# Optimization experiments

Hardware: AMD Instinct MI355X
Metric: run time of the kernel (lower is better)

## Reference

```python
import jax, jax.numpy as jnp
import numpy as np

B, S, D, H = 4, 2048, 1024, 16
DK = D // H

def setup_inputs() -> dict:
    key = jax.random.key(0)
    ks = jax.random.split(key, 8)
    scale = 1.0 / np.sqrt(D)
    return {
        "q": jax.random.normal(ks[0], (B, S, D), jnp.float32),
        "k": jax.random.normal(ks[1], (B, S, D), jnp.float32),
        "v": jax.random.normal(ks[2], (B, S, D), jnp.float32),
        "wq": jax.random.normal(ks[3], (D, D), jnp.float32) * scale,
        "bq": jnp.zeros((D,), jnp.float32),
        "wk": jax.random.normal(ks[4], (D, D), jnp.float32) * scale,
        "bk": jnp.zeros((D,), jnp.float32),
        "wv": jax.random.normal(ks[5], (D, D), jnp.float32) * scale,
        "bv": jnp.zeros((D,), jnp.float32),
        "wo": jax.random.normal(ks[6], (D, D), jnp.float32) * scale,
        "bo": jnp.zeros((D,), jnp.float32),
    }

def reference(q, k, v, wq, bq, wk, bk, wv, bv, wo, bo):
    b, s, _ = q.shape
    # projections; split heads -> [b, h, s, d_k]
    def proj(x, w, bias):
        y = x @ w + bias
        return y.reshape(b, -1, H, DK).transpose(0, 2, 1, 3)
    qh, kh, vh = proj(q, wq, bq), proj(k, wk, bk), proj(v, wv, bv)
    scores = jnp.einsum("bhqd,bhkd->bhqk", qh, kh) / np.sqrt(DK).astype(jnp.float32)
    attn = jax.nn.softmax(scores, axis=-1)  # dropout = identity (eval mode)
    out = jnp.einsum("bhqk,bhkd->bhqd", attn, vh)
    out = out.transpose(0, 2, 1, 3).reshape(b, s, D)
    return out @ wo + bo
```

## Files before the change

kernel.cpp:

```cpp
#include <hip/hip_runtime.h>
#include <hip/hip_bf16.h>

#define B_   4
#define S_   2048
#define D_   1024
#define H_   16
#define DK_  64
#define NTOK 8192

typedef __bf16 bf16_t;
typedef __bf16 bf16x8 __attribute__((ext_vector_type(8)));
typedef __bf16 bf16x4 __attribute__((ext_vector_type(4)));
typedef __bf16 bf16x2 __attribute__((ext_vector_type(2)));
typedef float  f32x4  __attribute__((ext_vector_type(4)));
typedef float  f32x16 __attribute__((ext_vector_type(16)));
typedef unsigned u32x4 __attribute__((ext_vector_type(4)));
typedef int    i32x2  __attribute__((ext_vector_type(2)));

__device__ __forceinline__ void gll16(const void* g, void* l) {
  __builtin_amdgcn_global_load_lds(
      (const __attribute__((address_space(1))) void*)g,
      (__attribute__((address_space(3))) void*)l,
      16, 0, 0);
}

__device__ __forceinline__ f32x4 mfma32(bf16x8 a, bf16x8 b, f32x4 c) {
  return __builtin_amdgcn_mfma_f32_16x16x32_bf16(a, b, c, 0, 0, 0);
}

__device__ __forceinline__ f32x16 mfma32x32(bf16x8 a, bf16x8 b, f32x16 c) {
#if defined(__HIP_DEVICE_COMPILE__)
  return __builtin_amdgcn_mfma_f32_32x32x16_bf16(a, b, c, 0, 0, 0);
#else
  (void)a; (void)b;
  return c;
#endif
}

__device__ __forceinline__ float fast_exp2(float x) {
#if defined(__HIP_DEVICE_COMPILE__) && __has_builtin(__builtin_amdgcn_exp2f)
  return __builtin_amdgcn_exp2f(x);
#else
  return exp2f(x);
#endif
}

__device__ __forceinline__ f32x16 zero16() {
  f32x16 z;
#pragma unroll
  for (int i = 0; i < 16; ++i) z[i] = 0.f;
  return z;
}

__device__ __forceinline__ unsigned pkbf(float lo, float hi) {
  bf16x2 t;
  t[0] = (bf16_t)lo;
  t[1] = (bf16_t)hi;
  return __builtin_bit_cast(unsigned, t);
}

__device__ __forceinline__ void plswap(unsigned &x, unsigned &y) {
#if defined(__HIP_DEVICE_COMPILE__)
  i32x2 r = __builtin_amdgcn_permlane32_swap((int)x, (int)y, false, false);
  x = (unsigned)r[0];
  y = (unsigned)r[1];
#endif
}

__device__ __forceinline__ void build_pa(const f32x16 s, bf16x8 &p0, bf16x8 &p1) {
  unsigned A0 = pkbf(fast_exp2(s[0]),  fast_exp2(s[1]));
  unsigned A1 = pkbf(fast_exp2(s[2]),  fast_exp2(s[3]));
  unsigned B0 = pkbf(fast_exp2(s[4]),  fast_exp2(s[5]));
  unsigned B1 = pkbf(fast_exp2(s[6]),  fast_exp2(s[7]));
  unsigned C0 = pkbf(fast_exp2(s[8]),  fast_exp2(s[9]));
  unsigned C1 = pkbf(fast_exp2(s[10]), fast_exp2(s[11]));
  unsigned D0 = pkbf(fast_exp2(s[12]), fast_exp2(s[13]));
  unsigned D1 = pkbf(fast_exp2(s[14]), fast_exp2(s[15]));
  plswap(A0, B0);
  plswap(A1, B1);
  plswap(C0, D0);
  plswap(C1, D1);
  u32x4 lo = {A0, A1, B0, B1};
  u32x4 hi = {C0, C1, D0, D1};
  p0 = __builtin_bit_cast(bf16x8, lo);
  p1 = __builtin_bit_cast(bf16x8, hi);
}

__global__ __launch_bounds__(256) void tobf16(
    const float* __restrict__ q, const float* __restrict__ k,
    const float* __restrict__ v, bf16_t* __restrict__ o) {
  const float* src = (blockIdx.z == 0) ? q : (blockIdx.z == 1) ? k : v;
  bf16_t* dst = o + (size_t)blockIdx.z * 8388608;
  size_t i = ((size_t)blockIdx.x * 256 + threadIdx.x) * 4;
  float4 x = *(const float4*)&src[i];
  bf16x4 y;
  y[0] = (bf16_t)x.x; y[1] = (bf16_t)x.y;
  y[2] = (bf16_t)x.z; y[3] = (bf16_t)x.w;
  *(bf16x4*)&dst[i] = y;
}

__global__ __launch_bounds__(256) void prep_weights(
    const float* __restrict__ wq, const float* __restrict__ wk,
    const float* __restrict__ wv, const float* __restrict__ wo,
    bf16_t* __restrict__ wtHi) {
  const int z = blockIdx.z;
  const float* W = (z == 0) ? wq : (z == 1) ? wk : (z == 2) ? wv : wo;
  const int k0 = blockIdx.x * 64;
  const int n0 = blockIdx.y * 64;
  const int t = threadIdx.x;
  __shared__ float T[64][65];
#pragma unroll
  for (int rr = 0; rr < 4; ++rr) {
    int row = rr * 16 + (t >> 4);
    int cc = (t & 15) * 4;
    const float4 v = *(const float4*)&W[(size_t)(k0 + row) * D_ + n0 + cc];
    T[row][cc + 0] = v.x; T[row][cc + 1] = v.y;
    T[row][cc + 2] = v.z; T[row][cc + 3] = v.w;
  }
  __syncthreads();
  const int n = t >> 2;
  const int kc = (t & 3) * 16;
  bf16x8 h0, h1;
#pragma unroll
  for (int j = 0; j < 16; ++j) {
    float vv = T[kc + j][n];
    if (j < 8) h0[j] = (bf16_t)vv;
    else       h1[j - 8] = (bf16_t)vv;
  }
  size_t ofs = (size_t)z * 1048576 + (size_t)(n0 + n) * D_ + k0 + kc;
  *(bf16x8*)&wtHi[ofs] = h0; *(bf16x8*)&wtHi[ofs + 8] = h1;
}

__global__ __launch_bounds__(256) void gemm_qkv_bf16(
    const bf16_t* __restrict__ Abf,
    const float* __restrict__ bq, const float* __restrict__ bk,
    const float* __restrict__ bv,
    const bf16_t* __restrict__ wtHi, bf16_t* __restrict__ outQKV) {
  const int z = blockIdx.z;
  const bf16_t* A   = Abf + (size_t)z * 8388608;
  const float* bias = (z == 0) ? bq : (z == 1) ? bk : bv;
  const bf16_t* WHi = wtHi + (size_t)z * 1048576;
  bf16_t* Out = outQKV + (size_t)z * 8388608;

  const int row0 = blockIdx.x * 128;
  const int col0 = blockIdx.y * 128;
  const int t = threadIdx.x;
  const int w = t >> 6, L = t & 63;
  const int m = L & 15, g = L >> 4;

  __shared__ __align__(16) bf16_t As2[128 * 32];
  __shared__ __align__(16) bf16_t Whi_s[128 * 32];

  f32x4 acc[4][4];
#pragma unroll
  for (int i = 0; i < 4; ++i)
#pragma unroll
    for (int j = 0; j < 4; ++j) acc[i][j] = (f32x4){0.f, 0.f, 0.f, 0.f};

  const int aw0 = (w & 1) * 64;
  const int bw0 = (w >> 1) * 64;

  for (int kt = 0; kt < 32; ++kt) {
    const int k0 = kt * 32;
#pragma unroll
    for (int rr = 0; rr < 2; ++rr) {
      int lin16 = rr * 256 + t;
      int n = lin16 >> 2;
      int c = (lin16 & 3) ^ ((n >> 1) & 3);
      gll16(&A[(size_t)(row0 + n) * D_ + k0 + c * 8], &As2[rr * 2048 + w * 512]);
      gll16(&WHi[(size_t)(col0 + n) * D_ + k0 + c * 8], &Whi_s[rr * 2048 + w * 512]);
    }
    __syncthreads();

    bf16x8 af[4], wh[4];
#pragma unroll
    for (int it = 0; it < 4; ++it) {
      int row = aw0 + it * 16 + m;
      int sl = (g ^ ((m >> 1) & 3)) * 8;
      af[it] = *(const bf16x8*)&As2[row * 32 + sl];
    }
#pragma unroll
    for (int jt = 0; jt < 4; ++jt) {
      int n = bw0 + jt * 16 + m;
      int sl = (g ^ ((m >> 1) & 3)) * 8;
      wh[jt] = *(const bf16x8*)&Whi_s[n * 32 + sl];
    }
#pragma unroll
    for (int it = 0; it < 4; ++it)
#pragma unroll
      for (int jt = 0; jt < 4; ++jt)
        acc[it][jt] = mfma32(af[it], wh[jt], acc[it][jt]);
    __syncthreads();
  }
#pragma unroll
  for (int jt = 0; jt < 4; ++jt) {
    int col = col0 + bw0 + jt * 16 + m;
    float bcol = bias[col];
    int h = col >> 6, d = col & 63;
#pragma unroll
    for (int it = 0; it < 4; ++it) {
      if (z != 2) {
#pragma unroll
        for (int r = 0; r < 4; ++r) {
          int row = row0 + aw0 + it * 16 + g * 4 + r;
          int b = row >> 11, s = row & 2047;
          Out[((size_t)((b * H_ + h) * S_ + s)) * DK_ + d] =
              (bf16_t)(acc[it][jt][r] + bcol);
        }
      } else {
        int row = row0 + aw0 + it * 16 + g * 4;
        int b = row >> 11, s = row & 2047;
        bf16x4 p4;
#pragma unroll
        for (int r = 0; r < 4; ++r) p4[r] = (bf16_t)(acc[it][jt][r] + bcol);
        *(bf16x4*)&Out[((size_t)((b * H_ + h) * DK_ + d)) * S_ + s] = p4;
      }
    }
  }
}

__global__ __launch_bounds__(256) void gemm_qkv_f32(
    const float* __restrict__ Aq, const float* __restrict__ Ak,
    const float* __restrict__ Av,
    const float* __restrict__ bq, const float* __restrict__ bk,
    const float* __restrict__ bv,
    const bf16_t* __restrict__ wtHi, bf16_t* __restrict__ outQKV) {
  const int z = blockIdx.z;
  const float* A    = (z == 0) ? Aq : (z == 1) ? Ak : Av;
  const float* bias = (z == 0) ? bq : (z == 1) ? bk : bv;
  const bf16_t* WHi = wtHi + (size_t)z * 1048576;
  bf16_t* Out = outQKV + (size_t)z * 8388608;

  const int row0 = blockIdx.x * 128;
  const int col0 = blockIdx.y * 128;
  const int t = threadIdx.x;
  const int w = t >> 6, L = t & 63;
  const int m = L & 15, g = L >> 4;

  __shared__ __align__(16) float  As[128 * 32];
  __shared__ __align__(16) bf16_t Whi_s[128 * 32];

  f32x4 acc[4][4];
#pragma unroll
  for (int i = 0; i < 4; ++i)
#pragma unroll
    for (int j = 0; j < 4; ++j) acc[i][j] = (f32x4){0.f, 0.f, 0.f, 0.f};

  const int aw0 = (w & 1) * 64;
  const int bw0 = (w >> 1) * 64;

  for (int kt = 0; kt < 32; ++kt) {
    const int k0 = kt * 32;
#pragma unroll
    for (int rr = 0; rr < 4; ++rr) {
      int lin16 = rr * 256 + t;
      int row = lin16 >> 3;
      int c = (lin16 & 7) ^ (row & 7);
      gll16(&A[(size_t)(row0 + row) * D_ + k0 + c * 4], &As[rr * 1024 + w * 256]);
    }
#pragma unroll
    for (int rr = 0; rr < 2; ++rr) {
      int lin16 = rr * 256 + t;
      int n = lin16 >> 2;
      int c = (lin16 & 3) ^ ((n >> 1) & 3);
      gll16(&WHi[(size_t)(col0 + n) * D_ + k0 + c * 8], &Whi_s[rr * 2048 + w * 512]);
    }
    __syncthreads();

    bf16x8 af[4], wh[4];
#pragma unroll
    for (int it = 0; it < 4; ++it) {
      int row = aw0 + it * 16 + m;
      const f32x4* p = (const f32x4*)&As[row * 32];
      f32x4 x0 = p[(2 * g) ^ (m & 7)];
      f32x4 x1 = p[(2 * g + 1) ^ (m & 7)];
      bf16x8 a;
      a[0] = (bf16_t)x0.x; a[1] = (bf16_t)x0.y; a[2] = (bf16_t)x0.z; a[3] = (bf16_t)x0.w;
      a[4] = (bf16_t)x1.x; a[5] = (bf16_t)x1.y; a[6] = (bf16_t)x1.z; a[7] = (bf16_t)x1.w;
      af[it] = a;
    }
#pragma unroll
    for (int jt = 0; jt < 4; ++jt) {
      int n = bw0 + jt * 16 + m;
      int sl = (g ^ ((m >> 1) & 3)) * 8;
      wh[jt] = *(const bf16x8*)&Whi_s[n * 32 + sl];
    }
#pragma unroll
    for (int it = 0; it < 4; ++it)
#pragma unroll
      for (int jt = 0; jt < 4; ++jt)
        acc[it][jt] = mfma32(af[it], wh[jt], acc[it][jt]);
    __syncthreads();
  }
#pragma unroll
  for (int jt = 0; jt < 4; ++jt) {
    int col = col0 + bw0 + jt * 16 + m;
    float bcol = bias[col];
    int h = col >> 6, d = col & 63;
#pragma unroll
    for (int it = 0; it < 4; ++it) {
      if (z != 2) {
#pragma unroll
        for (int r = 0; r < 4; ++r) {
          int row = row0 + aw0 + it * 16 + g * 4 + r;
          int b = row >> 11, s = row & 2047;
          Out[((size_t)((b * H_ + h) * S_ + s)) * DK_ + d] =
              (bf16_t)(acc[it][jt][r] + bcol);
        }
      } else {
        int row = row0 + aw0 + it * 16 + g * 4;
        int b = row >> 11, s = row & 2047;
        bf16x4 p4;
#pragma unroll
        for (int r = 0; r < 4; ++r) p4[r] = (bf16_t)(acc[it][jt][r] + bcol);
        *(bf16x4*)&Out[((size_t)((b * H_ + h) * DK_ + d)) * S_ + s] = p4;
      }
    }
  }
}

__global__ __launch_bounds__(256, 2) void attn(
    const bf16_t* __restrict__ Qh, const bf16_t* __restrict__ Kh,
    const bf16_t* __restrict__ VhT, bf16_t* __restrict__ Ohi) {
  const int lin = blockIdx.y * 16 + blockIdx.x;
  const int swz = (lin & 7) * 128 + (lin >> 3);
  const int bh = swz >> 4;
  const int q0 = (swz & 15) * 128;

  const int t = threadIdx.x, w = t >> 6;
  const int lane = t & 63;
  const int lo5 = lane & 31, hi = lane >> 5;

  __shared__ __align__(16) bf16_t Ks[2][64 * 64];
  __shared__ __align__(16) bf16_t Vt[2][64 * 64];

  const size_t qbase = (size_t)bh * S_ * DK_;
  const size_t vbase = (size_t)bh * DK_ * S_;

  const int lin16a = t, lin16b = 256 + t;
  const int rowa = lin16a >> 3, rowb = lin16b >> 3;
  const int ca = (lin16a & 7) ^ (rowa & 7);
  const int cb = (lin16b & 7) ^ (rowb & 7);

#define STAGE(buf, kv0)                                                        \
  do {                                                                         \
    gll16(&Kh[qbase + (size_t)((kv0) + rowa) * DK_ + ca * 8],                  \
          &Ks[buf][w * 512]);                                                  \
    gll16(&VhT[vbase + (size_t)rowa * S_ + (kv0) + ca * 8],                    \
          &Vt[buf][w * 512]);                                                  \
    gll16(&Kh[qbase + (size_t)((kv0) + rowb) * DK_ + cb * 8],                  \
          &Ks[buf][2048 + w * 512]);                                           \
    gll16(&VhT[vbase + (size_t)rowb * S_ + (kv0) + cb * 8],                    \
          &Vt[buf][2048 + w * 512]);                                           \
  } while (0)

  STAGE(0, 0);

  const int qrow = q0 + w * 32 + lo5;
  bf16x8 qf[4];
#pragma unroll
  for (int ks = 0; ks < 4; ++ks) {
    bf16x8 v = *(const bf16x8*)&Qh[qbase + (size_t)qrow * DK_ + ks * 16 + hi * 8];
#pragma unroll
    for (int j = 0; j < 8; ++j) v[j] = (bf16_t)(0.18033688f * (float)v[j]);
    qf[ks] = v;
  }

  bf16x8 ones;
#pragma unroll
  for (int j = 0; j < 8; ++j) ones[j] = (bf16_t)1.f;

  int offs[4];
#pragma unroll
  for (int ks = 0; ks < 4; ++ks)
    offs[ks] = lo5 * 64 + (((ks * 2 + hi) ^ (lo5 & 7)) * 8);

  f32x16 oacc0 = zero16(), oacc1 = zero16(), lacc = zero16();

  __syncthreads();

  for (int it = 0; it < 32; ++it) {
    const int cur = it & 1;
    if (it < 31) STAGE(cur ^ 1, (it + 1) * 64);

    const bf16_t* ks_b = &Ks[cur][0];
    const bf16_t* vt_b = &Vt[cur][0];

    f32x16 sc0 = zero16(), sc1 = zero16();
#pragma unroll
    for (int ks = 0; ks < 4; ++ks) {
      bf16x8 k0 = *(const bf16x8*)&ks_b[offs[ks]];
      bf16x8 k1 = *(const bf16x8*)&ks_b[offs[ks] + 2048];
      sc0 = mfma32x32(k0, qf[ks], sc0);
      sc1 = mfma32x32(k1, qf[ks], sc1);
    }

    bf16x8 pa0, pa1, pa2, pa3;
    build_pa(sc0, pa0, pa1);
    build_pa(sc1, pa2, pa3);

#pragma unroll
    for (int ks = 0; ks < 4; ++ks) {
      bf16x8 pb = (ks == 0) ? pa0 : (ks == 1) ? pa1 : (ks == 2) ? pa2 : pa3;
      lacc = mfma32x32(ones, pb, lacc);
      bf16x8 v0 = *(const bf16x8*)&vt_b[offs[ks]];
      bf16x8 v1 = *(const bf16x8*)&vt_b[offs[ks] + 2048];
      oacc0 = mfma32x32(v0, pb, oacc0);
      oacc1 = mfma32x32(v1, pb, oacc1);
    }

    __syncthreads();
  }
#undef STAGE

  const int b = bh >> 4, h = bh & 15;
  const float inv = 1.f / lacc[0];
  const size_t rowofs = ((size_t)(b * S_ + qrow)) * D_ + h * DK_;
#pragma unroll
  for (int rg = 0; rg < 4; ++rg) {
    bf16x4 o0, o1;
#pragma unroll
    for (int j = 0; j < 4; ++j) {
      o0[j] = (bf16_t)(oacc0[rg * 4 + j] * inv);
      o1[j] = (bf16_t)(oacc1[rg * 4 + j] * inv);
    }
    *(bf16x4*)&Ohi[rowofs + rg * 8 + hi * 4] = o0;
    *(bf16x4*)&Ohi[rowofs + 32 + rg * 8 + hi * 4] = o1;
  }
}

__global__ __launch_bounds__(256) void gemm_out(
    const bf16_t* __restrict__ Ahi, const bf16_t* __restrict__ wtHi,
    const float* __restrict__ bias, float* __restrict__ Out) {
  const bf16_t* WHi = wtHi + (size_t)3 * 1048576;
  const int row0 = blockIdx.x * 128;
  const int col0 = blockIdx.y * 128;
  const int t = threadIdx.x;
  const int w = t >> 6, L = t & 63;
  const int m = L & 15, g = L >> 4;

  __shared__ __align__(16) bf16_t Ahi_s[128 * 32];
  __shared__ __align__(16) bf16_t Whi_s[128 * 32];

  f32x4 acc[4][4];
#pragma unroll
  for (int i = 0; i < 4; ++i)
#pragma unroll
    for (int j = 0; j < 4; ++j) acc[i][j] = (f32x4){0.f, 0.f, 0.f, 0.f};

  const int aw0 = (w & 1) * 64;
  const int bw0 = (w >> 1) * 64;

  for (int kt = 0; kt < 32; ++kt) {
    const int k0 = kt * 32;
#pragma unroll
    for (int rr = 0; rr < 2; ++rr) {
      int lin16 = rr * 256 + t;
      int n = lin16 >> 2;
      int c = (lin16 & 3) ^ ((n >> 1) & 3);
      gll16(&Ahi[(size_t)(row0 + n) * D_ + k0 + c * 8], &Ahi_s[rr * 2048 + w * 512]);
      gll16(&WHi[(size_t)(col0 + n) * D_ + k0 + c * 8], &Whi_s[rr * 2048 + w * 512]);
    }
    __syncthreads();

    bf16x8 ah[4], wh[4];
#pragma unroll
    for (int it = 0; it < 4; ++it) {
      int row = aw0 + it * 16 + m;
      int sl = (g ^ ((m >> 1) & 3)) * 8;
      ah[it] = *(const bf16x8*)&Ahi_s[row * 32 + sl];
    }
#pragma unroll
    for (int jt = 0; jt < 4; ++jt) {
      int n = bw0 + jt * 16 + m;
      int sl = (g ^ ((m >> 1) & 3)) * 8;
      wh[jt] = *(const bf16x8*)&Whi_s[n * 32 + sl];
    }
#pragma unroll
    for (int it = 0; it < 4; ++it)
#pragma unroll
      for (int jt = 0; jt < 4; ++jt)
        acc[it][jt] = mfma32(ah[it], wh[jt], acc[it][jt]);
    __syncthreads();
  }
#pragma unroll
  for (int jt = 0; jt < 4; ++jt) {
    int col = col0 + bw0 + jt * 16 + m;
    float bcol = bias[col];
#pragma unroll
    for (int it = 0; it < 4; ++it)
#pragma unroll
      for (int r = 0; r < 4; ++r) {
        int row = row0 + aw0 + it * 16 + g * 4 + r;
        Out[(size_t)row * D_ + col] = acc[it][jt][r] + bcol;
      }
  }
}

extern "C" void kernel_launch(void* const* d_in, const int* in_sizes, int n_in,
                              void* d_out, int out_size, void* d_ws, size_t ws_size,
                              hipStream_t stream) {
  const float* q  = (const float*)d_in[0];
  const float* k  = (const float*)d_in[1];
  const float* v  = (const float*)d_in[2];
  const float* wq = (const float*)d_in[3];
  const float* bq = (const float*)d_in[4];
  const float* wk = (const float*)d_in[5];
  const float* bk = (const float*)d_in[6];
  const float* wv = (const float*)d_in[7];
  const float* bv = (const float*)d_in[8];
  const float* wo = (const float*)d_in[9];
  const float* bo = (const float*)d_in[10];
  float* out = (float*)d_out;

  char* ws = (char*)d_ws;
  bf16_t* wtHi = (bf16_t*)(ws);
  bf16_t* QKVh = (bf16_t*)(ws + (8ull << 20));
  bf16_t* Ohi  = (bf16_t*)(ws + (56ull << 20));
  bf16_t* Abf  = (bf16_t*)(ws + (56ull << 20));

  const bool big = ws_size >= (104ull << 20);

  hipLaunchKernelGGL(prep_weights, dim3(16, 16, 4), dim3(256), 0, stream,
                     wq, wk, wv, wo, wtHi);
  if (big) {
    hipLaunchKernelGGL(tobf16, dim3(8192, 1, 3), dim3(256), 0, stream,
                       q, k, v, Abf);
    hipLaunchKernelGGL(gemm_qkv_bf16, dim3(64, 8, 3), dim3(256), 0, stream,
                       Abf, bq, bk, bv, wtHi, QKVh);
  } else {
    hipLaunchKernelGGL(gemm_qkv_f32, dim3(64, 8, 3), dim3(256), 0, stream,
                       q, k, v, bq, bk, bv, wtHi, QKVh);
  }
  hipLaunchKernelGGL(attn, dim3(16, 64), dim3(256), 0, stream,
                     QKVh, QKVh + 8388608, QKVh + 16777216, Ohi);
  hipLaunchKernelGGL(gemm_out, dim3(64, 8), dim3(256), 0, stream,
                     Ohi, wtHi, bo, out);
}
```

Baseline: 348.6 us.

## Software-pipeline attention loop: overlap PV of previous tile with QK of current

Restructures the attention main loop so each iteration computes the QK scores for the current KV tile while issuing the PV MFMAs for the previous tile, with V fragments preloaded into registers. The double buffer is split into separate named arrays and the loop is unrolled by two so buffer addresses are static. s_setprio raises wave priority around the MFMA bursts so waves alternate between matrix work and softmax/LDS work. This adds register pressure from holding pa and vr across iterations, which could hurt occupancy under launch_bounds(256,2).

Result: no change. 344.4 us (-1.2%).

```diff
diff --git a/kernel.cpp b/kernel.cpp
--- a/kernel.cpp
+++ b/kernel.cpp
@@ -331,8 +331,10 @@
   const int lane = t & 63;
   const int lo5 = lane & 31, hi = lane >> 5;
 
-  __shared__ __align__(16) bf16_t Ks[2][64 * 64];
-  __shared__ __align__(16) bf16_t Vt[2][64 * 64];
+  __shared__ __align__(16) bf16_t Ks0[64 * 64];
+  __shared__ __align__(16) bf16_t Ks1[64 * 64];
+  __shared__ __align__(16) bf16_t Vt0[64 * 64];
+  __shared__ __align__(16) bf16_t Vt1[64 * 64];
 
   const size_t qbase = (size_t)bh * S_ * DK_;
   const size_t vbase = (size_t)bh * DK_ * S_;
@@ -342,19 +344,19 @@
   const int ca = (lin16a & 7) ^ (rowa & 7);
   const int cb = (lin16b & 7) ^ (rowb & 7);
 
-#define STAGE(buf, kv0)                                                        \
+#define STAGE2(KsD, VtD, kv0)                                                  \
   do {                                                                         \
     gll16(&Kh[qbase + (size_t)((kv0) + rowa) * DK_ + ca * 8],                  \
-          &Ks[buf][w * 512]);                                                  \
+          &KsD[w * 512]);                                                      \
     gll16(&VhT[vbase + (size_t)rowa * S_ + (kv0) + ca * 8],                    \
-          &Vt[buf][w * 512]);                                                  \
+          &VtD[w * 512]);                                                      \
     gll16(&Kh[qbase + (size_t)((kv0) + rowb) * DK_ + cb * 8],                  \
-          &Ks[buf][2048 + w * 512]);                                           \
+          &KsD[2048 + w * 512]);                                               \
     gll16(&VhT[vbase + (size_t)rowb * S_ + (kv0) + cb * 8],                    \
-          &Vt[buf][2048 + w * 512]);                                           \
+          &VtD[2048 + w * 512]);                                               \
   } while (0)
 
-  STAGE(0, 0);
+  STAGE2(Ks0, Vt0, 0);
 
   const int qrow = q0 + w * 32 + lo5;
   bf16x8 qf[4];
@@ -376,42 +378,67 @@
     offs[ks] = lo5 * 64 + (((ks * 2 + hi) ^ (lo5 & 7)) * 8);
 
   f32x16 oacc0 = zero16(), oacc1 = zero16(), lacc = zero16();
+  bf16x8 pa[4];
+  bf16x8 vr[8];
 
   __syncthreads();
 
-  for (int it = 0; it < 32; ++it) {
-    const int cur = it & 1;
-    if (it < 31) STAGE(cur ^ 1, (it + 1) * 64);
-
-    const bf16_t* ks_b = &Ks[cur][0];
-    const bf16_t* vt_b = &Vt[cur][0];
-
-    f32x16 sc0 = zero16(), sc1 = zero16();
-#pragma unroll
-    for (int ks = 0; ks < 4; ++ks) {
-      bf16x8 k0 = *(const bf16x8*)&ks_b[offs[ks]];
-      bf16x8 k1 = *(const bf16x8*)&ks_b[offs[ks] + 2048];
-      sc0 = mfma32x32(k0, qf[ks], sc0);
-      sc1 = mfma32x32(k1, qf[ks], sc1);
-    }
-
-    bf16x8 pa0, pa1, pa2, pa3;
-    build_pa(sc0, pa0, pa1);
-    build_pa(sc1, pa2, pa3);
-
-#pragma unroll
-    for (int ks = 0; ks < 4; ++ks) {
-      bf16x8 pb = (ks == 0) ? pa0 : (ks == 1) ? pa1 : (ks == 2) ? pa2 : pa3;
-      lacc = mfma32x32(ones, pb, lacc);
-      bf16x8 v0 = *(const bf16x8*)&vt_b[offs[ks]];
-      bf16x8 v1 = *(const bf16x8*)&vt_b[offs[ks] + 2048];
-      oacc0 = mfma32x32(v0, pb, oacc0);
-      oacc1 = mfma32x32(v1, pb, oacc1);
-    }
-
-    __syncthreads();
-  }
-#undef STAGE
+#define ATTN_BODY(KsC, VtC, DO_PV)                                             \
+  do {                                                                         \
+    f32x16 sc0 = zero16(), sc1 = zero16();                                     \
+    __builtin_amdgcn_s_setprio(1);                                             \
+    _Pragma("unroll")                                                          \
+    for (int ks = 0; ks < 4; ++ks) {                                           \
+      bf16x8 k0 = *(const bf16x8*)&KsC[offs[ks]];                              \
+      bf16x8 k1 = *(const bf16x8*)&KsC[offs[ks] + 2048];                       \
+      sc0 = mfma32x32(k0, qf[ks], sc0);                                        \
+      sc1 = mfma32x32(k1, qf[ks], sc1);                                        \
+    }                                                                          \
+    if (DO_PV) {                                                               \
+      _Pragma("unroll")                                                        \
+      for (int ks = 0; ks < 4; ++ks) {                                         \
+        lacc  = mfma32x32(ones, pa[ks], lacc);                                 \
+        oacc0 = mfma32x32(vr[2 * ks], pa[ks], oacc0);                          \
+        oacc1 = mfma32x32(vr[2 * ks + 1], pa[ks], oacc1);                      \
+      }                                                                        \
+    }                                                                          \
+    __builtin_amdgcn_s_setprio(0);                                             \
+    _Pragma("unroll")                                                          \
+    for (int ks = 0; ks < 4; ++ks) {                                           \
+      vr[2 * ks]     = *(const bf16x8*)&VtC[offs[ks]];                         \
+      vr[2 * ks + 1] = *(const bf16x8*)&VtC[offs[ks] + 2048];                  \
+    }                                                                          \
+    build_pa(sc0, pa[0], pa[1]);                                               \
+    build_pa(sc1, pa[2], pa[3]);                                               \
+  } while (0)
+
+  STAGE2(Ks1, Vt1, 64);
+  ATTN_BODY(Ks0, Vt0, false);
+  __syncthreads();
+
+  for (int tp = 0; tp < 15; ++tp) {
+    const int kv1 = (2 * tp + 2) * 64;
+    const int kv2 = (2 * tp + 3) * 64;
+    STAGE2(Ks0, Vt0, kv1);
+    ATTN_BODY(Ks1, Vt1, true);
+    __syncthreads();
+    STAGE2(Ks1, Vt1, kv2);
+    ATTN_BODY(Ks0, Vt0, true);
+    __syncthreads();
+  }
+
+  ATTN_BODY(Ks1, Vt1, true);
+
+  __builtin_amdgcn_s_setprio(1);
+#pragma unroll
+  for (int ks = 0; ks < 4; ++ks) {
+    lacc  = mfma32x32(ones, pa[ks], lacc);
+    oacc0 = mfma32x32(vr[2 * ks], pa[ks], oacc0);
+    oacc1 = mfma32x32(vr[2 * ks + 1], pa[ks], oacc1);
+  }
+  __builtin_amdgcn_s_setprio(0);
+#undef ATTN_BODY
+#undef STAGE2
 
   const int b = bh >> 4, h = bh & 15;
   const float inv = 1.f / lacc[0];
```
